# Optimization experiments

Measured on AMD Instinct MI355X. Metric: run time of the kernel, lower is better.

The kernel has to match this reference:

```python
import jax, jax.numpy as jnp
import numpy as np

B, S, D = 2, 2048, 1024
H = 16
HD = D // H  # 64
SCALE = HD ** 0.5


def setup_inputs() -> dict:
    key = jax.random.key(0)
    ks = jax.random.split(key, 7)
    return {
        "query": jax.random.normal(ks[0], (B, S, D), dtype=jnp.float32),
        "key": jax.random.normal(ks[1], (B, S, D), dtype=jnp.float32),
        "value": jax.random.normal(ks[2], (B, S, D), dtype=jnp.float32),
        "W_qkv_w": jax.random.normal(ks[3], (3 * D, 3 * D), dtype=jnp.float32) * (1.0 / np.sqrt(3 * D)),
        "W_qkv_b": jax.random.normal(ks[4], (3 * D,), dtype=jnp.float32) * 0.02,
        "W_o_w": jax.random.normal(ks[5], (D, D), dtype=jnp.float32) * (1.0 / np.sqrt(D)),
        "W_o_b": jax.random.normal(ks[6], (D,), dtype=jnp.float32) * 0.02,
    }


def _split_heads(x):
    # [B,S,D] -> [B,H,S,HD]
    return x.reshape(B, S, H, HD).transpose(0, 2, 1, 3)


def reference(query, key, value, W_qkv_w, W_qkv_b, W_o_w, W_o_b):
    # fused QKV projection: concat then Linear(3D, 3D)  (torch: x @ W.T + b)
    qkv = jnp.concatenate([query, key, value], axis=-1)
    qkv = qkv @ W_qkv_w.T + W_qkv_b
    q, k, v = jnp.split(qkv, 3, axis=-1)
    q, k, v = _split_heads(q), _split_heads(k), _split_heads(v)
    # naive attention: materializes [B,H,S,S]
    scores = jnp.einsum('bhqd,bhkd->bhqk', q, k) / SCALE
    probs = jax.nn.softmax(scores, axis=-1)
    attn = jnp.einsum('bhqk,bhkd->bhqd', probs, v)
    # combine heads: [B,H,S,HD] -> [B,S,D]
    attn = attn.transpose(0, 2, 1, 3).reshape(B, S, D)
    return attn @ W_o_w.T + W_o_b
```

## Files before the change

kernel.cpp:

```cpp
#include <hip/hip_runtime.h>
#include <cmath>

#define BS   2
#define SEQ  2048
#define DM   1024
#define NH   16
#define HD   64
#define D3   3072
#define MROWS 4096
#define KVBLK 64
#define QBLK  128
#define NTILES (SEQ / KVBLK)

#define CSC 0.18033688011112042f

typedef _Float16 f16;
typedef __attribute__((ext_vector_type(4))) _Float16 half4;
typedef __attribute__((ext_vector_type(8))) _Float16 half8;
typedef __attribute__((ext_vector_type(4))) float f32x4;
typedef unsigned int u32;
typedef __attribute__((ext_vector_type(2))) u32 u32x2;
typedef __attribute__((ext_vector_type(4))) u32 u32x4;

__device__ __forceinline__ void async_cp16(const void* g, void* s) {
    __builtin_amdgcn_global_load_lds(
        (const __attribute__((address_space(1))) u32*)g,
        (__attribute__((address_space(3))) u32*)s, 16, 0, 0);
}

__global__ __launch_bounds__(256) void conv_concat_kernel(
    const float* __restrict__ q, const float* __restrict__ k,
    const float* __restrict__ v, f16* __restrict__ out)
{
    const int seg = blockIdx.x;
    const int row = blockIdx.y;
    const int c   = threadIdx.x * 4;
    const float* src = (seg == 0 ? q : (seg == 1 ? k : v)) + (size_t)row * DM + c;
    float4 x = *(const float4*)src;
    half4 h = {(f16)x.x, (f16)x.y, (f16)x.z, (f16)x.w};
    *(half4*)&out[(size_t)row * D3 + seg * DM + c] = h;
}

__global__ __launch_bounds__(256) void conv_plain_kernel(
    const float* __restrict__ src, f16* __restrict__ dst, int n4)
{
    int i = blockIdx.x * 256 + threadIdx.x;
    const int stride = gridDim.x * 256;
    for (; i < n4; i += stride) {
        float4 x = *(const float4*)&src[(size_t)i * 4];
        half4 h = {(f16)x.x, (f16)x.y, (f16)x.z, (f16)x.w};
        *(half4*)&dst[(size_t)i * 4] = h;
    }
}

#define SWZ4(r) (((r) >> 1) & 3)

template<int KDIM, int NDIM>
__global__ __launch_bounds__(512, 2) void gemm8p_f16_kernel(
    const f16* __restrict__ A, const f16* __restrict__ W,
    const float* __restrict__ bias, f16* __restrict__ Cout)
{
    __shared__ f16 lds[65536];

    const int tid  = threadIdx.x;
    const int lane = tid & 63;
    const int wave = tid >> 6;
    const int l15  = lane & 15;
    const int lg   = lane >> 4;
    const int wm   = wave >> 2;
    const int wn   = wave & 3;

    const int cpx = gridDim.x >> 3;
    const int lid = (blockIdx.x & 7) * cpx + (blockIdx.x >> 3);
    const int NTC = NDIM / 256;
    const int tM0 = (lid / NTC) * 256;
    const int tN0 = (lid % NTC) * 256;

    const int rr  = wave * 16 + (lane >> 2);
    const int cs  = (lane & 3) ^ SWZ4(rr);
    const f16* gA = A + (size_t)(tM0 + rr) * KDIM + cs * 8;
    const f16* gW = W + (size_t)(tN0 + rr) * KDIM + cs * 8;
    const int sbase = wave * 512;

    f32x4 acc[8][4];
#pragma unroll
    for (int i = 0; i < 8; ++i)
#pragma unroll
        for (int j = 0; j < 4; ++j) acc[i][j] = (f32x4){0.f, 0.f, 0.f, 0.f};

    const int fch = lg ^ SWZ4(l15);
    const int aro = (wm * 128 + l15) * 32 + fch * 8;
    const int bro = 32768 + (wn * 64 + l15) * 32 + fch * 8;

    constexpr int NT = KDIM / 64;

#define STAGE_A(S, KS, KT) do {                                               \
    const f16* s_ = gA + (size_t)(KT) * 64 + (KS) * 32;                       \
    f16* d_ = &lds[(S) * 16384 + (KS) * 8192 + sbase];                        \
    async_cp16(s_, d_);                                                       \
    async_cp16(s_ + (size_t)128 * KDIM, d_ + 4096);                           \
} while (0)

#define STAGE_B(S, KS, KT) do {                                               \
    const f16* s_ = gW + (size_t)(KT) * 64 + (KS) * 32;                       \
    f16* d_ = &lds[32768 + (S) * 16384 + (KS) * 8192 + sbase];                \
    async_cp16(s_, d_);                                                       \
    async_cp16(s_ + (size_t)128 * KDIM, d_ + 4096);                           \
} while (0)

#define PHASE(S, KS, MH, VMEND, STAGE_STMT) do {                              \
    const int pb_ = (S) * 16384 + (KS) * 8192;                                \
    half8 af[4];                                                              \
    _Pragma("unroll")                                                         \
    for (int mi = 0; mi < 4; ++mi)                                            \
        af[mi] = *(half8*)&lds[pb_ + aro + ((MH) * 4 + mi) * 512];            \
    if ((MH) == 0) {                                                          \
        _Pragma("unroll")                                                     \
        for (int ni = 0; ni < 4; ++ni)                                        \
            wf[ni] = *(half8*)&lds[pb_ + bro + ni * 512];                     \
    }                                                                         \
    STAGE_STMT;                                                               \
    __builtin_amdgcn_s_barrier();                                             \
    asm volatile("s_waitcnt lgkmcnt(0)" ::: "memory");                        \
    __builtin_amdgcn_sched_barrier(0);                                        \
    __builtin_amdgcn_s_setprio(1);                                            \
    _Pragma("unroll")                                                         \
    for (int mi = 0; mi < 4; ++mi)                                            \
        _Pragma("unroll")                                                     \
        for (int ni = 0; ni < 4; ++ni)                                        \
            acc[(MH) * 4 + mi][ni] = __builtin_amdgcn_mfma_f32_16x16x32_f16(  \
                af[mi], wf[ni], acc[(MH) * 4 + mi][ni], 0, 0, 0);             \
    __builtin_amdgcn_s_setprio(0);                                            \
    __builtin_amdgcn_sched_barrier(0);                                        \
    if (VMEND) {                                                              \
        asm volatile("s_waitcnt vmcnt(8)" ::: "memory");                      \
        __builtin_amdgcn_sched_barrier(0);                                    \
    }                                                                         \
    __builtin_amdgcn_s_barrier();                                             \
} while (0)

    STAGE_A(0, 0, 0); STAGE_B(0, 0, 0);
    STAGE_A(0, 1, 0); STAGE_B(0, 1, 0);
    STAGE_A(1, 0, 1); STAGE_B(1, 0, 1);
    asm volatile("s_waitcnt vmcnt(8)" ::: "memory");
    __builtin_amdgcn_s_barrier();

    half8 wf[4];
    for (int it = 0; it < NT / 2; ++it) {
        const int t   = 2 * it;
        const int t1c = t + 1;
        const int t2c = (t + 2 < NT) ? t + 2 : NT - 1;
        const int t3c = (t + 3 < NT) ? t + 3 : NT - 1;
        PHASE(0, 0, 0, false, STAGE_A(1, 1, t1c));
        PHASE(0, 0, 1, true,  STAGE_B(1, 1, t1c));
        PHASE(0, 1, 0, false, STAGE_A(0, 0, t2c));
        PHASE(0, 1, 1, true,  STAGE_B(0, 0, t2c));
        PHASE(1, 0, 0, false, STAGE_A(0, 1, t2c));
        PHASE(1, 0, 1, true,  STAGE_B(0, 1, t2c));
        PHASE(1, 1, 0, false, STAGE_A(1, 0, t3c));
        PHASE(1, 1, 1, true,  STAGE_B(1, 0, t3c));
    }

#undef PHASE
#undef STAGE_A
#undef STAGE_B

    float bv[4];
#pragma unroll
    for (int ni = 0; ni < 4; ++ni) bv[ni] = bias[tN0 + wn * 64 + ni * 16 + l15];

#pragma unroll
    for (int mi = 0; mi < 8; ++mi)
#pragma unroll
        for (int ni = 0; ni < 4; ++ni)
#pragma unroll
            for (int r = 0; r < 4; ++r) {
                const int m   = tM0 + wm * 128 + mi * 16 + lg * 4 + r;
                const int col = tN0 + wn * 64 + ni * 16 + l15;
                Cout[(size_t)m * NDIM + col] = (f16)(acc[mi][ni][r] + bv[ni]);
            }
}

__global__ __launch_bounds__(128) void gemm_out_kernel(
    const f16* __restrict__ A, const f16* __restrict__ W,
    const float* __restrict__ bias, float* __restrict__ Cout)
{
    constexpr int KDIM = DM, NDIM = DM;
    __shared__ f16 As[64 * 32];
    __shared__ f16 Ws[128 * 32];

    const int tid  = threadIdx.x;
    const int lane = tid & 63;
    const int wave = tid >> 6;
    const int l15  = lane & 15;
    const int lg   = lane >> 4;

    const int cpx = gridDim.x >> 3;
    const int lid = (blockIdx.x & 7) * cpx + (blockIdx.x >> 3);
    const int NT2 = NDIM / 128;
    const int tM0 = (lid / NT2) * 64;
    const int tN0 = (lid % NT2) * 128;

    const int srow = lane >> 2;
    const int sch  = lane & 3;
    const int ssc  = sch ^ ((srow >> 1) & 3);

    const f16* gA0 = A + (size_t)(tM0 + wave * 32      + srow) * KDIM + ssc * 8;
    const f16* gA1 = A + (size_t)(tM0 + wave * 32 + 16 + srow) * KDIM + ssc * 8;
    const f16* gW0 = W + (size_t)(tN0 + wave * 64      + srow) * KDIM + ssc * 8;
    const f16* gW1 = W + (size_t)(tN0 + wave * 64 + 16 + srow) * KDIM + ssc * 8;
    const f16* gW2 = W + (size_t)(tN0 + wave * 64 + 32 + srow) * KDIM + ssc * 8;
    const f16* gW3 = W + (size_t)(tN0 + wave * 64 + 48 + srow) * KDIM + ssc * 8;
    f16* lA0 = &As[(wave * 32)      * 32];
    f16* lA1 = &As[(wave * 32 + 16) * 32];
    f16* lW0 = &Ws[(wave * 64)      * 32];
    f16* lW1 = &Ws[(wave * 64 + 16) * 32];
    f16* lW2 = &Ws[(wave * 64 + 32) * 32];
    f16* lW3 = &Ws[(wave * 64 + 48) * 32];

    f32x4 acc[4][4];
#pragma unroll
    for (int i = 0; i < 4; ++i)
#pragma unroll
        for (int j = 0; j < 4; ++j) acc[i][j] = (f32x4){0.f, 0.f, 0.f, 0.f};

    const int fsw = (lg ^ ((l15 >> 1) & 3)) * 8;
    int aoff[4], woff[4];
#pragma unroll
    for (int mi = 0; mi < 4; ++mi) aoff[mi] = (mi * 16 + l15) * 32 + fsw;
#pragma unroll
    for (int ni = 0; ni < 4; ++ni) woff[ni] = (wave * 64 + ni * 16 + l15) * 32 + fsw;

    for (int k0 = 0; k0 < KDIM; k0 += 32) {
        __syncthreads();
        async_cp16(gA0 + k0, lA0);
        async_cp16(gA1 + k0, lA1);
        async_cp16(gW0 + k0, lW0);
        async_cp16(gW1 + k0, lW1);
        async_cp16(gW2 + k0, lW2);
        async_cp16(gW3 + k0, lW3);
        __syncthreads();

        half8 af[4], wf[4];
#pragma unroll
        for (int mi = 0; mi < 4; ++mi) af[mi] = *(half8*)&As[aoff[mi]];
#pragma unroll
        for (int ni = 0; ni < 4; ++ni) wf[ni] = *(half8*)&Ws[woff[ni]];
#pragma unroll
        for (int mi = 0; mi < 4; ++mi)
#pragma unroll
            for (int ni = 0; ni < 4; ++ni)
                acc[mi][ni] = __builtin_amdgcn_mfma_f32_16x16x32_f16(
                    af[mi], wf[ni], acc[mi][ni], 0, 0, 0);
    }

    float bv[4];
#pragma unroll
    for (int ni = 0; ni < 4; ++ni) bv[ni] = bias[tN0 + wave * 64 + ni * 16 + l15];

#pragma unroll
    for (int mi = 0; mi < 4; ++mi)
#pragma unroll
        for (int ni = 0; ni < 4; ++ni)
#pragma unroll
            for (int r = 0; r < 4; ++r) {
                const int m   = tM0 + mi * 16 + lg * 4 + r;
                const int col = tN0 + wave * 64 + ni * 16 + l15;
                Cout[(size_t)m * NDIM + col] = acc[mi][ni][r] + bv[ni];
            }
}


#define V_STORE(VtN, va, vb) do {                                             \
    u32x4 aw_ = __builtin_bit_cast(u32x4, va);                                \
    u32x4 bw_ = __builtin_bit_cast(u32x4, vb);                                \
    _Pragma("unroll")                                                         \
    for (int wd_ = 0; wd_ < 4; ++wd_) {                                       \
        u32 lo_ = __builtin_amdgcn_perm(bw_[wd_], aw_[wd_], 0x05040100u);     \
        u32 hi_ = __builtin_amdgcn_perm(bw_[wd_], aw_[wd_], 0x07060302u);     \
        const int dl_ = vd0 + 2 * wd_;                                        \
        const int dh_ = dl_ + 1;                                              \
        *(u32*)&VtN[dl_ * KVBLK + (((vp >> 2) ^ (dl_ & 7) ^ (dl_ >> 3)) * 8)  \
                    + 2 * (vp & 3)] = lo_;                                    \
        *(u32*)&VtN[dh_ * KVBLK + (((vp >> 2) ^ (dh_ & 7) ^ (dh_ >> 3)) * 8)  \
                    + 2 * (vp & 3)] = hi_;                                    \
    }                                                                         \
} while (0)

#define ATTN_STEP(KhC, VtC, KhN, VtN, TT, PF) do {                            \
    half8 va_ = {}, vb_ = {};                                                 \
    if (PF) {                                                                 \
        const size_t nro_ = (size_t)((TT) + 1) * KVBLK;                       \
        async_cp16(kxsrc + (nro_ + wave * 16 +     krow_l) * D3,              \
                   &KhN[(wave * 16) * HD]);                                   \
        async_cp16(kxsrc + (nro_ + wave * 16 + 8 + krow_l) * D3,              \
                   &KhN[(wave * 16 + 8) * HD]);                               \
        va_ = *(const half8*)(vsrc0 + nro_ * D3);                             \
        vb_ = *(const half8*)(vsrc0 + nro_ * D3 + D3);                        \
    }                                                                         \
    f32x4 sc[2][4];                                                           \
    _Pragma("unroll")                                                         \
    for (int rt = 0; rt < 2; ++rt)                                            \
        _Pragma("unroll")                                                     \
        for (int ct = 0; ct < 4; ++ct) sc[rt][ct] = (f32x4){0.f,0.f,0.f,0.f}; \
    __builtin_amdgcn_s_setprio(1);                                            \
    _Pragma("unroll")                                                         \
    for (int ct = 0; ct < 4; ++ct) {                                          \
        const int krow = ct * 16 + l15;                                       \
        _Pragma("unroll")                                                     \
        for (int ks = 0; ks < 2; ++ks) {                                      \
            half8 kf = *(half8*)&KhC[krow * HD +                              \
                                     (((ks * 4 + lg) ^ (krow & 7)) * 8)];     \
            _Pragma("unroll")                                                 \
            for (int rt = 0; rt < 2; ++rt)                                    \
                sc[rt][ct] = __builtin_amdgcn_mfma_f32_16x16x32_f16(          \
                    kf, qf[rt][ks], sc[rt][ct], 0, 0, 0);                     \
        }                                                                     \
    }                                                                         \
    __builtin_amdgcn_s_setprio(0);                                            \
    _Pragma("unroll")                                                         \
    for (int rt = 0; rt < 2; ++rt) {                                          \
        float mt = sc[rt][0][0];                                              \
        _Pragma("unroll")                                                     \
        for (int ct = 0; ct < 4; ++ct)                                        \
            _Pragma("unroll")                                                 \
            for (int r = 0; r < 4; ++r)                                       \
                if (ct || r) mt = fmaxf(mt, sc[rt][ct][r]);                   \
        mt = fmaxf(mt, __shfl_xor(mt, 16));                                   \
        mt = fmaxf(mt, __shfl_xor(mt, 32));                                   \
        const float mn = fmaxf(mrun[rt], mt * CSC);                           \
        const float alpha = exp2f(mrun[rt] - mn);                             \
        mrun[rt] = mn;                                                        \
        float pv_[4][4];                                                      \
        float ls = 0.f;                                                       \
        _Pragma("unroll")                                                     \
        for (int ct = 0; ct < 4; ++ct)                                        \
            _Pragma("unroll")                                                 \
            for (int r = 0; r < 4; ++r) {                                     \
                pv_[ct][r] = exp2f(fmaf(sc[rt][ct][r], CSC, -mn));            \
                ls += pv_[ct][r];                                             \
            }                                                                 \
        ls += __shfl_xor(ls, 16);                                             \
        ls += __shfl_xor(ls, 32);                                             \
        lrun[rt] = lrun[rt] * alpha + ls;                                     \
        _Pragma("unroll")                                                     \
        for (int dct = 0; dct < 4; ++dct)                                     \
            _Pragma("unroll")                                                 \
            for (int r = 0; r < 4; ++r) oacc[rt][dct][r] *= alpha;            \
        const int prow_ = pbase + (rt * 16 + l15) * KVBLK;                    \
        _Pragma("unroll")                                                     \
        for (int ct = 0; ct < 4; ++ct) {                                      \
            u32 w01 = __builtin_bit_cast(u32,                                 \
                __builtin_amdgcn_cvt_pkrtz(pv_[ct][0], pv_[ct][1]));          \
            u32 w23 = __builtin_bit_cast(u32,                                 \
                __builtin_amdgcn_cvt_pkrtz(pv_[ct][2], pv_[ct][3]));          \
            *(u32x2*)&Pl[prow_ + ((4 * ct + lg) ^ l15) * 4] =                 \
                (u32x2){w01, w23};                                            \
        }                                                                     \
    }                                                                         \
    __builtin_amdgcn_s_setprio(1);                                            \
    _Pragma("unroll")                                                         \
    for (int ks2 = 0; ks2 < 2; ++ks2) {                                       \
        half8 pa[2];                                                          \
        _Pragma("unroll")                                                     \
        for (int rt = 0; rt < 2; ++rt) {                                      \
            const int prow_ = pbase + (rt * 16 + l15) * KVBLK;                \
            half4 plA_ = *(half4*)&Pl[prow_ + ((8 * ks2 + 2 * lg)     ^ l15) * 4]; \
            half4 plB_ = *(half4*)&Pl[prow_ + ((8 * ks2 + 2 * lg + 1) ^ l15) * 4]; \
            pa[rt] = __builtin_shufflevector(plA_, plB_, 0,1,2,3,4,5,6,7);    \
        }                                                                     \
        _Pragma("unroll")                                                     \
        for (int dct = 0; dct < 4; ++dct) {                                   \
            const int d = dct * 16 + l15;                                     \
            half8 vf = *(half8*)&VtC[d * KVBLK +                              \
                        (((ks2 * 4 + lg) ^ (d & 7) ^ (d >> 3)) * 8)];         \
            _Pragma("unroll")                                                 \
            for (int rt = 0; rt < 2; ++rt)                                    \
                oacc[rt][dct] = __builtin_amdgcn_mfma_f32_16x16x32_f16(       \
                    vf, pa[rt], oacc[rt][dct], 0, 0, 0);                      \
        }                                                                     \
    }                                                                         \
    __builtin_amdgcn_s_setprio(0);                                            \
    if (PF) { V_STORE(VtN, va_, vb_); }                                       \
    __syncthreads();                                                          \
} while (0)

__global__ __launch_bounds__(256, 2) void attn_mfma_kernel(
    const f16* __restrict__ qkvh, f16* __restrict__ attnh)
{
    __shared__ f16 Kh0[KVBLK * HD];
    __shared__ f16 Kh1[KVBLK * HD];
    __shared__ f16 Vt0[HD * KVBLK];
    __shared__ f16 Vt1[HD * KVBLK];
    __shared__ f16 Pl[4 * 32 * KVBLK];

    const int tid  = threadIdx.x;
    const int lane = tid & 63;
    const int wave = tid >> 6;
    const int l15  = lane & 15;
    const int lg   = lane >> 4;

    const int nq  = SEQ / QBLK;
    const int cpx = gridDim.x >> 3;
    const int lid = (blockIdx.x & 7) * cpx + (blockIdx.x >> 3);
    const int b   = lid / (NH * nq);
    const int h   = (lid / nq) % NH;
    const int qc  = lid % nq;
    const int q0  = qc * QBLK + wave * 32;
    const size_t bS = (size_t)b * SEQ;

    const int krow_l = lane >> 3;
    const int kschk  = (lane & 7) ^ krow_l;
    const f16* kxsrc = qkvh + bS * D3 + DM + h * HD + kschk * 8;

    const int vp  = tid >> 3;
    const int vd0 = (tid & 7) * 8;
    const f16* vsrc0 = qkvh + (bS + 2 * vp) * D3 + 2 * DM + h * HD + vd0;

    half8 qf[2][2];
#pragma unroll
    for (int rt = 0; rt < 2; ++rt)
#pragma unroll
        for (int ks = 0; ks < 2; ++ks)
            qf[rt][ks] = *(const half8*)&qkvh[(bS + q0 + rt * 16 + l15) * D3 +
                                              h * HD + ks * 32 + lg * 8];

    f32x4 oacc[2][4];
#pragma unroll
    for (int rt = 0; rt < 2; ++rt)
#pragma unroll
        for (int dct = 0; dct < 4; ++dct) oacc[rt][dct] = (f32x4){0.f, 0.f, 0.f, 0.f};

    float mrun[2], lrun[2];
#pragma unroll
    for (int rt = 0; rt < 2; ++rt) { mrun[rt] = -INFINITY; lrun[rt] = 0.f; }

    const int pbase = wave * 32 * KVBLK;

    {
        async_cp16(kxsrc + (size_t)(wave * 16 +     krow_l) * D3, &Kh0[(wave * 16) * HD]);
        async_cp16(kxsrc + (size_t)(wave * 16 + 8 + krow_l) * D3, &Kh0[(wave * 16 + 8) * HD]);
        half8 va_ = *(const half8*)(vsrc0);
        half8 vb_ = *(const half8*)(vsrc0 + D3);
        V_STORE(Vt0, va_, vb_);
        __syncthreads();
    }

    for (int t = 0; t < NTILES; t += 2) {
        ATTN_STEP(Kh0, Vt0, Kh1, Vt1, t, true);
        ATTN_STEP(Kh1, Vt1, Kh0, Vt0, t + 1, (t + 1) < (NTILES - 1));
    }

#pragma unroll
    for (int rt = 0; rt < 2; ++rt) {
        const float inv = 1.f / lrun[rt];
        const int qq = q0 + rt * 16 + l15;
#pragma unroll
        for (int dct = 0; dct < 4; ++dct) {
            half4 o;
#pragma unroll
            for (int r = 0; r < 4; ++r) o[r] = (f16)(oacc[rt][dct][r] * inv);
            *(half4*)&attnh[(bS + qq) * DM + h * HD + dct * 16 + 4 * lg] = o;
        }
    }
}

extern "C" void kernel_launch(void* const* d_in, const int* in_sizes, int n_in,
                              void* d_out, int out_size, void* d_ws, size_t ws_size,
                              hipStream_t stream) {
    const float* q    = (const float*)d_in[0];
    const float* k    = (const float*)d_in[1];
    const float* v    = (const float*)d_in[2];
    const float* Wqkv = (const float*)d_in[3];
    const float* bqkv = (const float*)d_in[4];
    const float* Wo   = (const float*)d_in[5];
    const float* bo   = (const float*)d_in[6];
    float* out = (float*)d_out;

    char* ws = (char*)d_ws;
    f16* Ain    = (f16*)ws;
    f16* attn_h = (f16*)ws;
    f16* Wo_h   = (f16*)(ws + 16777216);
    f16* Wqkv_h = (f16*)(ws + 25165824);
    f16* qkv_h  = (f16*)(ws + 44040192);

    conv_concat_kernel<<<dim3(3, MROWS), 256, 0, stream>>>(q, k, v, Ain);
    conv_plain_kernel<<<2048, 256, 0, stream>>>(Wqkv, Wqkv_h, D3 * D3 / 4);

    gemm8p_f16_kernel<D3, D3><<<dim3((MROWS / 256) * (D3 / 256)), 512, 0, stream>>>(
        Ain, Wqkv_h, bqkv, qkv_h);

    attn_mfma_kernel<<<dim3(BS * NH * (SEQ / QBLK)), 256, 0, stream>>>(qkv_h, attn_h);

    conv_plain_kernel<<<512, 256, 0, stream>>>(Wo, Wo_h, DM * DM / 4);

    gemm_out_kernel<<<dim3((MROWS / 64) * (DM / 128)), 128, 0, stream>>>(
        attn_h, Wo_h, bo, out);
}
```

Before: 196.4 us.

## Split attention KV range into two chunks and merge with a combine kernel

The attention kernel now splits each (batch, head, query-block) into two halves of the key/value sequence. This doubles the grid so more blocks are resident per CU. Each chunk writes its unnormalized fp16 output plus its running max and sum to workspace. A new combine kernel rescales and merges the two partial results before the output projection. In exchange it adds an extra kernel launch and extra global traffic for the partial outputs, and the unnormalized partials are stored at fp16 precision.

```diff
diff --git a/kernel.cpp b/kernel.cpp
--- a/kernel.cpp
+++ b/kernel.cpp
@@ -11,6 +11,8 @@
 #define KVBLK 64
 #define QBLK  128
 #define NTILES (SEQ / KVBLK)
+#define NCHUNK 2
+#define CTILES (NTILES / NCHUNK)
 
 #define CSC 0.18033688011112042f
 
@@ -386,7 +388,7 @@
 } while (0)
 
 __global__ __launch_bounds__(256, 2) void attn_mfma_kernel(
-    const f16* __restrict__ qkvh, f16* __restrict__ attnh)
+    const f16* __restrict__ qkvh, f16* __restrict__ U, float2* __restrict__ ml)
 {
     __shared__ f16 Kh0[KVBLK * HD];
     __shared__ f16 Kh1[KVBLK * HD];
@@ -403,11 +405,16 @@
     const int nq  = SEQ / QBLK;
     const int cpx = gridDim.x >> 3;
     const int lid = (blockIdx.x & 7) * cpx + (blockIdx.x >> 3);
-    const int b   = lid / (NH * nq);
-    const int h   = (lid / nq) % NH;
-    const int qc  = lid % nq;
-    const int q0  = qc * QBLK + wave * 32;
+    const int qc = lid % nq;
+    const int hc = lid / nq;
+    const int c  = hc & (NCHUNK - 1);
+    const int bh = hc / NCHUNK;
+    const int h  = bh % NH;
+    const int b  = bh / NH;
+    const int q0 = qc * QBLK + wave * 32;
     const size_t bS = (size_t)b * SEQ;
+    const int t0 = c * CTILES;
+    const int tEnd = t0 + CTILES;
 
     const int krow_l = lane >> 3;
     const int kschk  = (lane & 7) ^ krow_l;
@@ -438,31 +445,62 @@
     const int pbase = wave * 32 * KVBLK;
 
     {
-        async_cp16(kxsrc + (size_t)(wave * 16 +     krow_l) * D3, &Kh0[(wave * 16) * HD]);
-        async_cp16(kxsrc + (size_t)(wave * 16 + 8 + krow_l) * D3, &Kh0[(wave * 16 + 8) * HD]);
-        half8 va_ = *(const half8*)(vsrc0);
-        half8 vb_ = *(const half8*)(vsrc0 + D3);
+        const size_t r0 = (size_t)t0 * KVBLK;
+        async_cp16(kxsrc + (r0 + wave * 16 +     krow_l) * D3, &Kh0[(wave * 16) * HD]);
+        async_cp16(kxsrc + (r0 + wave * 16 + 8 + krow_l) * D3, &Kh0[(wave * 16 + 8) * HD]);
+        half8 va_ = *(const half8*)(vsrc0 + r0 * D3);
+        half8 vb_ = *(const half8*)(vsrc0 + r0 * D3 + D3);
         V_STORE(Vt0, va_, vb_);
         __syncthreads();
     }
 
-    for (int t = 0; t < NTILES; t += 2) {
+    for (int t = t0; t < tEnd; t += 2) {
         ATTN_STEP(Kh0, Vt0, Kh1, Vt1, t, true);
-        ATTN_STEP(Kh1, Vt1, Kh0, Vt0, t + 1, (t + 1) < (NTILES - 1));
+        ATTN_STEP(Kh1, Vt1, Kh0, Vt0, t + 1, (t + 2) < tEnd);
     }
 
+    f16* Uc = U + (size_t)c * MROWS * DM;
 #pragma unroll
     for (int rt = 0; rt < 2; ++rt) {
-        const float inv = 1.f / lrun[rt];
         const int qq = q0 + rt * 16 + l15;
 #pragma unroll
         for (int dct = 0; dct < 4; ++dct) {
             half4 o;
 #pragma unroll
-            for (int r = 0; r < 4; ++r) o[r] = (f16)(oacc[rt][dct][r] * inv);
-            *(half4*)&attnh[(bS + qq) * DM + h * HD + dct * 16 + 4 * lg] = o;
+            for (int r = 0; r < 4; ++r) o[r] = (f16)oacc[rt][dct][r];
+            *(half4*)&Uc[(bS + qq) * DM + h * HD + dct * 16 + 4 * lg] = o;
         }
+        if (lg == 0)
+            ml[(((size_t)c * BS + b) * NH + h) * SEQ + qq] =
+                make_float2(mrun[rt], lrun[rt]);
     }
+}
+
+__global__ __launch_bounds__(128) void attn_combine_kernel(
+    const f16* __restrict__ U, const float2* __restrict__ ml,
+    f16* __restrict__ outh)
+{
+    const int row = blockIdx.x;
+    const int b = row >> 11;
+    const int q = row & (SEQ - 1);
+    const int d = threadIdx.x * 8;
+    const int h = d >> 6;
+
+    const float2 a1 = ml[(((size_t)0 * BS + b) * NH + h) * SEQ + q];
+    const float2 a2 = ml[(((size_t)1 * BS + b) * NH + h) * SEQ + q];
+    const float m  = fmaxf(a1.x, a2.x);
+    float w1 = exp2f(a1.x - m);
+    float w2 = exp2f(a2.x - m);
+    const float inv = 1.f / (a1.y * w1 + a2.y * w2);
+    w1 *= inv; w2 *= inv;
+
+    half8 u1 = *(const half8*)&U[(size_t)row * DM + d];
+    half8 u2 = *(const half8*)&U[(size_t)(MROWS + row) * DM + d];
+    half8 o;
+#pragma unroll
+    for (int e = 0; e < 8; ++e)
+        o[e] = (f16)((float)u1[e] * w1 + (float)u2[e] * w2);
+    *(half8*)&outh[(size_t)row * DM + d] = o;
 }
 
 extern "C" void kernel_launch(void* const* d_in, const int* in_sizes, int n_in,
@@ -479,8 +517,10 @@
 
     char* ws = (char*)d_ws;
     f16* Ain    = (f16*)ws;
+    f16* U      = (f16*)ws;
     f16* attn_h = (f16*)ws;
     f16* Wo_h   = (f16*)(ws + 16777216);
+    float2* ml  = (float2*)(ws + 20971520);
     f16* Wqkv_h = (f16*)(ws + 25165824);
     f16* qkv_h  = (f16*)(ws + 44040192);
 
@@ -490,9 +530,12 @@
     gemm8p_f16_kernel<D3, D3><<<dim3((MROWS / 256) * (D3 / 256)), 512, 0, stream>>>(
         Ain, Wqkv_h, bqkv, qkv_h);
 
-    attn_mfma_kernel<<<dim3(BS * NH * (SEQ / QBLK)), 256, 0, stream>>>(qkv_h, attn_h);
+    attn_mfma_kernel<<<dim3(BS * NH * (SEQ / QBLK) * NCHUNK), 256, 0, stream>>>(
+        qkv_h, U, ml);
 
     conv_plain_kernel<<<512, 256, 0, stream>>>(Wo, Wo_h, DM * DM / 4);
+
+    attn_combine_kernel<<<dim3(MROWS), 128, 0, stream>>>(U, ml, attn_h);
 
     gemm_out_kernel<<<dim3((MROWS / 64) * (DM / 128)), 128, 0, stream>>>(
         attn_h, Wo_h, bo, out);
```

Result: slower. 203.8 us (+3.7%).
